# Optimization experiments

Measured on AMD Instinct MI355X. Metric: run time of the kernel, lower is better.

## Reference

```python
import jax, jax.numpy as jnp
import numpy as np

B, C, H, W = 8, 256, 128, 128
G = 32            # n_groups
CPG = C // G      # channels per group = 8
K = 3             # adaptive spatial kernel and final conv kernel
OUT = 256         # out_channels of final conv
EPS = 1e-5
DN = ('NCHW', 'OIHW', 'NCHW')


def setup_inputs() -> dict:
    key = jax.random.key(0)
    ks = jax.random.split(key, 6)
    x = jax.random.normal(ks[0], (B, C, H, W), jnp.float32)
    w_spatial = jax.random.normal(ks[1], (B, C, CPG, K, K), jnp.float32) * 0.05
    w_pointwise = jax.random.normal(ks[2], (B, C, CPG, 1, 1), jnp.float32) * 0.05
    bias = jax.random.normal(ks[3], (B, C), jnp.float32) * 0.05
    # learned params of the final (static) conv
    conv_w = jax.random.normal(ks[4], (OUT, C, K, K), jnp.float32) * 0.05
    conv_b = jax.random.normal(ks[5], (OUT,), jnp.float32) * 0.05
    return {'x': x, 'w_spatial': w_spatial, 'w_pointwise': w_pointwise,
            'bias': bias, 'conv_w': conv_w, 'conv_b': conv_b}


def _ada_single(x, ws, wp, b):
    # x: [C,H,W]; ws: [C,CPG,K,K]; wp: [C,CPG,1,1]; b: [C]
    pad = (K - 1) // 2
    xp = jnp.pad(x, ((0, 0), (pad, pad), (pad, pad)), mode='reflect')
    # grouped spatial conv (channel-preserving)
    y = jax.lax.conv_general_dilated(
        xp[None], ws, (1, 1), 'VALID',
        dimension_numbers=DN, feature_group_count=G)[0]      # [C,H,W]
    # grouped 1x1 conv as per-group small matmul
    yg = y.reshape(G, CPG, H, W)
    wg = wp[:, :, 0, 0].reshape(G, CPG, CPG)                 # [G, out/g, in/g]
    z = jnp.einsum('goi,gihw->gohw', wg, yg).reshape(C, H, W)
    return z + b[:, None, None]


def reference(x, w_spatial, w_pointwise, bias, conv_w, conv_b):
    # instance norm (no affine), biased variance as in F.instance_norm
    mean = x.mean(axis=(2, 3), keepdims=True)
    var = x.var(axis=(2, 3), keepdims=True)
    xn = (x - mean) * jax.lax.rsqrt(var + EPS)
    # per-sample adaptive depthwise-separable conv
    y = jax.vmap(_ada_single)(xn, w_spatial, w_pointwise, bias)  # [B,C,H,W]
    # final static conv, reflect padding (ceil,floor) = (1,1) for k=3
    yp = jnp.pad(y, ((0, 0), (0, 0), (1, 1), (1, 1)), mode='reflect')
    out = jax.lax.conv_general_dilated(yp, conv_w, (1, 1), 'VALID',
                                       dimension_numbers=DN)
    return out + conv_b[None, :, None, None]
```

## Files before the change

kernel.cpp:

```cpp
#include <hip/hip_runtime.h>
#include <stdint.h>
#include <stddef.h>


typedef __attribute__((ext_vector_type(8))) short   s16x8;
typedef __attribute__((ext_vector_type(4))) float   f32x4;

#define NB   8
#define NC   256
#define NH   128
#define NW   128
#define NG   32
#define CPG  8
#define NOUT 256
#define HWPLANE (NH*NW)

__device__ __forceinline__ unsigned short f2bf(float f) {
    union { float f; unsigned u; } v; v.f = f;
    unsigned u = v.u;
    u += 0x7fffu + ((u >> 16) & 1u);
    return (unsigned short)(u >> 16);
}

__device__ __forceinline__ int refl128(int i) {
    return i < 0 ? 1 : (i > 127 ? 126 : i);
}

__device__ __forceinline__ void async_load16(const void* g, void* l) {
    __builtin_amdgcn_global_load_lds(
        (const __attribute__((address_space(1))) unsigned int*)g,
        (__attribute__((address_space(3))) unsigned int*)l,
        16, 0, 0);
}

__global__ __launch_bounds__(256) void stats_k(const float* __restrict__ x,
                                               float* __restrict__ stats) {
    int bc = blockIdx.x, t = threadIdx.x;
    const float4* p = (const float4*)(x + (size_t)bc * HWPLANE);
    float s = 0.f, q = 0.f;
#pragma unroll
    for (int k = 0; k < 16; ++k) {
        float4 v = p[k * 256 + t];
        s += v.x + v.y + v.z + v.w;
        q += v.x * v.x + v.y * v.y + v.z * v.z + v.w * v.w;
    }
    __shared__ float ss[256], sq[256];
    ss[t] = s; sq[t] = q;
    __syncthreads();
    for (int o = 128; o > 0; o >>= 1) {
        if (t < o) { ss[t] += ss[t + o]; sq[t] += sq[t + o]; }
        __syncthreads();
    }
    if (t == 0) {
        float mean = ss[0] * (1.f / HWPLANE);
        float var  = sq[0] * (1.f / HWPLANE) - mean * mean;
        stats[bc * 2]     = mean;
        stats[bc * 2 + 1] = rsqrtf(var + 1e-5f);
    }
}

__global__ __launch_bounds__(256) void weff_k(const float* __restrict__ wsp,
                                              const float* __restrict__ wpw,
                                              float* __restrict__ weff) {
    int tid = blockIdx.x * 256 + threadIdx.x;
    int e  = tid % 72;
    int bc = tid / 72;
    int c = bc & 255, b = bc >> 8, g = c >> 3;
    int i = e / 9, t = e - i * 9;
    float acc = 0.f;
#pragma unroll
    for (int j = 0; j < 8; ++j)
        acc += wpw[bc * 8 + j] * wsp[(((b * NC + g * 8 + j) * CPG) + i) * 9 + t];
    weff[(size_t)bc * 72 + e] = acc;
}

__global__ __launch_bounds__(256) void repack_k(const float* __restrict__ cw,
                                                unsigned short* __restrict__ wtT) {
    int tid = blockIdx.x * 256 + threadIdx.x;
    int c = tid & 255;
    int o = (tid >> 8) & 255;
    int t = tid >> 16;
    float v = cw[(size_t)(o * NC + c) * 9 + t];
    wtT[((size_t)t * NOUT + o) * NC + c] = f2bf(v);
}

__global__ __launch_bounds__(128) void ada_k(const float* __restrict__ x,
                                             const float* __restrict__ stats,
                                             const float* __restrict__ weff,
                                             const float* __restrict__ bias,
                                             unsigned short* __restrict__ z) {
    int bx = blockIdx.x;
    int h = bx & 127;
    int g = (bx >> 7) & 31;
    int b = bx >> 12;
    int w = threadIdx.x;

    __shared__ float sx[CPG][3][NW];
#pragma unroll
    for (int ic = 0; ic < CPG; ++ic) {
        int cg = g * 8 + ic;
        float mean = stats[(b * NC + cg) * 2];
        float rstd = stats[(b * NC + cg) * 2 + 1];
        const float* xp = x + (size_t)(b * NC + cg) * HWPLANE;
#pragma unroll
        for (int dh = 0; dh < 3; ++dh) {
            int r = refl128(h + dh - 1);
            sx[ic][dh][w] = (xp[r * NW + w] - mean) * rstd;
        }
    }
    __syncthreads();

    float acc[CPG];
    const float* bp = bias + b * NC + g * 8;
#pragma unroll
    for (int c = 0; c < CPG; ++c) acc[c] = bp[c];

    const float* wp = weff + (size_t)(b * NC + g * 8) * 72;
    int wm = (w == 0) ? 1 : w - 1;
    int wq = (w == 127) ? 126 : w + 1;

#pragma unroll
    for (int ic = 0; ic < CPG; ++ic) {
        float xv[9];
#pragma unroll
        for (int dh = 0; dh < 3; ++dh) {
            xv[dh * 3 + 0] = sx[ic][dh][wm];
            xv[dh * 3 + 1] = sx[ic][dh][w];
            xv[dh * 3 + 2] = sx[ic][dh][wq];
        }
#pragma unroll
        for (int c = 0; c < CPG; ++c)
#pragma unroll
            for (int t = 0; t < 9; ++t)
                acc[c] += wp[c * 72 + ic * 9 + t] * xv[t];
    }

    unsigned short ob[8];
#pragma unroll
    for (int c = 0; c < CPG; ++c) ob[c] = f2bf(acc[c]);
    uint4 pk;
    pk.x = (unsigned)ob[0] | ((unsigned)ob[1] << 16);
    pk.y = (unsigned)ob[2] | ((unsigned)ob[3] << 16);
    pk.z = (unsigned)ob[4] | ((unsigned)ob[5] << 16);
    pk.w = (unsigned)ob[6] | ((unsigned)ob[7] << 16);
    *(uint4*)(z + ((size_t)((b * NH + h) * NW + w)) * NC + g * 8) = pk;
}

__global__ __launch_bounds__(256, 3) void final_k(const unsigned short* __restrict__ z,
                                                  const unsigned short* __restrict__ wtT,
                                                  const float* __restrict__ cb,
                                                  float* __restrict__ out) {
    __shared__ s16x8 sAv[1024];
    __shared__ s16x8 sBv[2][1024];

    const int id = blockIdx.x;
    const int b  = id & 7;
    const int jb = id >> 3;
    const int nb = jb & 1;
    const int h  = jb >> 1;

    const int tid  = threadIdx.x;
    const int wv   = tid >> 6;
    const int lane = tid & 63;
    const int l15  = lane & 15;
    const int quad = lane >> 4;
    const int mo   = (wv & 1) << 6;
    const int nol  = (wv >> 1) << 6;
    const int n0   = (nb << 7) + nol;

    int srcoff[4], ldsoff[4];
#pragma unroll
    for (int it = 0; it < 4; ++it) {
        int ch  = it * 256 + tid;
        int row = ch >> 3, cp = ch & 7;
        srcoff[it] = row * 512 + ((cp ^ (row & 7)) << 4);
        ldsoff[it] = it * 256 + wv * 64;
    }

    int aoff[3][4][2];
#pragma unroll
    for (int dw = 0; dw < 3; ++dw)
#pragma unroll
        for (int i = 0; i < 4; ++i) {
            int w_ = refl128(mo + 16 * i + l15 + dw - 1);
#pragma unroll
            for (int kk = 0; kk < 2; ++kk)
                aoff[dw][i][kk] = w_ * 8 + ((kk * 4 + quad) ^ (w_ & 7));
        }
    int boff[4][2];
#pragma unroll
    for (int j = 0; j < 4; ++j) {
        int oc_l = nol + 16 * j + l15;
#pragma unroll
        for (int kk = 0; kk < 2; ++kk)
            boff[j][kk] = oc_l * 8 + ((kk * 4 + quad) ^ (oc_l & 7));
    }

    const char* zb = (const char*)z + (size_t)b * (HWPLANE * NC * 2);
    const char* zr[3];
#pragma unroll
    for (int dh = 0; dh < 3; ++dh)
        zr[dh] = zb + (size_t)refl128(h + dh - 1) * (NW * NC * 2);
    const char* wt = (const char*)wtT + nb * 65536;

    auto stageA = [&](const char* g) {
#pragma unroll
        for (int it = 0; it < 4; ++it)
            async_load16(g + srcoff[it], (void*)(sAv + ldsoff[it]));
    };
    auto stageB = [&](const char* g, int bsel) {
#pragma unroll
        for (int it = 0; it < 4; ++it)
            async_load16(g + srcoff[it], (void*)(sBv[bsel] + ldsoff[it]));
    };

    f32x4 acc[4][4] = {};

    auto compute = [&](const int (&ao)[4][2], int bsel) {
        const s16x8* bbase = sBv[bsel];
#pragma unroll
        for (int kk = 0; kk < 2; ++kk) {
            s16x8 av[4], bv[4];
#pragma unroll
            for (int i = 0; i < 4; ++i) av[i] = sAv[ao[i][kk]];
#pragma unroll
            for (int j = 0; j < 4; ++j) bv[j] = bbase[boff[j][kk]];
#pragma unroll
            for (int i = 0; i < 4; ++i)
#pragma unroll
                for (int j = 0; j < 4; ++j)
                    acc[i][j] = __builtin_amdgcn_mfma_f32_16x16x32_bf16(
                        av[i], bv[j], acc[i][j], 0, 0, 0);
        }
    };

    int buf = 0;
    stageA(zr[0]);
    stageB(wt, 0);
    __syncthreads();

    for (int sc = 0; sc < 12; ++sc) {
        const int dh = sc >> 2, kc = sc & 3;
        const char* bt = wt + (size_t)(dh * 3) * 131072 + kc * 128;
        stageB(bt + 131072, buf ^ 1);
        compute(aoff[0], buf);
        __syncthreads(); buf ^= 1;
        stageB(bt + 262144, buf ^ 1);
        compute(aoff[1], buf);
        __syncthreads(); buf ^= 1;
        compute(aoff[2], buf);
        __syncthreads();
        if (sc < 11) {
            const int sn = sc + 1, dhn = sn >> 2, kcn = sn & 3;
            stageA(zr[dhn] + kcn * 128);
            stageB(wt + (size_t)(dhn * 3) * 131072 + kcn * 128, buf ^ 1);
            __syncthreads();
        }
        buf ^= 1;
    }

#pragma unroll
    for (int j = 0; j < 4; ++j) {
        int oc = n0 + 16 * j + l15;
        float bvl = cb[oc];
#pragma unroll
        for (int i = 0; i < 4; ++i) {
            int w0 = mo + 16 * i + quad * 4;
            float* dst = out + (((size_t)(b * NOUT + oc) * NH + h) * NW + w0);
            f32x4 v = acc[i][j];
            float4 o4 = { v[0] + bvl, v[1] + bvl, v[2] + bvl, v[3] + bvl };
            *(float4*)dst = o4;
        }
    }
}

extern "C" void kernel_launch(void* const* d_in, const int* in_sizes, int n_in,
                              void* d_out, int out_size, void* d_ws, size_t ws_size,
                              hipStream_t stream) {
    const float* x   = (const float*)d_in[0];
    const float* wsp = (const float*)d_in[1];
    const float* wpw = (const float*)d_in[2];
    const float* bia = (const float*)d_in[3];
    const float* cw  = (const float*)d_in[4];
    const float* cb  = (const float*)d_in[5];
    float* out = (float*)d_out;

    char* ws = (char*)d_ws;
    float*          stats = (float*)ws;
    float*          weff  = (float*)(ws + 16384);
    unsigned short* wtT   = (unsigned short*)(ws + 606208);
    unsigned short* z     = (unsigned short*)(ws + 1785856);

    stats_k <<<NB * NC, 256, 0, stream>>>(x, stats);
    weff_k  <<<576,     256, 0, stream>>>(wsp, wpw, weff);
    repack_k<<<2304,    256, 0, stream>>>(cw, wtT);
    ada_k   <<<NB * NG * NH, 128, 0, stream>>>(x, stats, weff, bia, z);
    final_k <<<NB * NH * 2,  256, 0, stream>>>(z, wtT, cb, out);
}
```

Measured before the change: 501.2 us.

## Tile adaptive conv over 8 rows per block with register-blocked rows and reordered weights

The adaptive grouped conv kernel now handles an 8-row tile per 256-thread block instead of one row per 128-thread block. It loads 10 halo rows into shared memory with float4 loads, and each thread computes 4 output rows for 8 output channels. Each loaded input value is reused across 3 vertical taps and 4 rows, which cuts redundant halo reads from global memory. The effective-weight layout is transposed to [ic][tap][oc] so the 8 output-channel weights are contiguous. The cost is higher register use (32 accumulators) and larger shared memory per block.

```diff
diff --git a/kernel.cpp b/kernel.cpp
--- a/kernel.cpp
+++ b/kernel.cpp
@@ -63,15 +63,17 @@
                                               const float* __restrict__ wpw,
                                               float* __restrict__ weff) {
     int tid = blockIdx.x * 256 + threadIdx.x;
-    int e  = tid % 72;
-    int bc = tid / 72;
-    int c = bc & 255, b = bc >> 8, g = c >> 3;
-    int i = e / 9, t = e - i * 9;
+    int oc = tid & 7;
+    int q  = tid >> 3;
+    int t  = q % 9;
+    int q2 = q / 9;
+    int ic = q2 & 7;
+    int bg = q2 >> 3;
     float acc = 0.f;
 #pragma unroll
     for (int j = 0; j < 8; ++j)
-        acc += wpw[bc * 8 + j] * wsp[(((b * NC + g * 8 + j) * CPG) + i) * 9 + t];
-    weff[(size_t)bc * 72 + e] = acc;
+        acc += wpw[(bg * 8 + oc) * 8 + j] * wsp[((bg * 8 + j) * 8 + ic) * 9 + t];
+    weff[(size_t)((bg * 8 + ic) * 9 + t) * 8 + oc] = acc;
 }
 
 __global__ __launch_bounds__(256) void repack_k(const float* __restrict__ cw,
@@ -84,66 +86,83 @@
     wtT[((size_t)t * NOUT + o) * NC + c] = f2bf(v);
 }
 
-__global__ __launch_bounds__(128) void ada_k(const float* __restrict__ x,
+__global__ __launch_bounds__(256) void ada_k(const float* __restrict__ x,
                                              const float* __restrict__ stats,
                                              const float* __restrict__ weff,
                                              const float* __restrict__ bias,
                                              unsigned short* __restrict__ z) {
-    int bx = blockIdx.x;
-    int h = bx & 127;
-    int g = (bx >> 7) & 31;
-    int b = bx >> 12;
-    int w = threadIdx.x;
-
-    __shared__ float sx[CPG][3][NW];
-#pragma unroll
-    for (int ic = 0; ic < CPG; ++ic) {
-        int cg = g * 8 + ic;
+    __shared__ float sx[CPG][10][NW];
+    const int bx = blockIdx.x;
+    const int ht = bx & 15;
+    const int g  = (bx >> 4) & 31;
+    const int b  = bx >> 9;
+    const int h0 = ht * 8;
+
+#pragma unroll
+    for (int it = 0; it < 10; ++it) {
+        int p   = it * 256 + threadIdx.x;
+        int ic  = p / 320;
+        int rem = p - ic * 320;
+        int row = rem >> 5;
+        int w4  = rem & 31;
+        int cg  = g * 8 + ic;
         float mean = stats[(b * NC + cg) * 2];
         float rstd = stats[(b * NC + cg) * 2 + 1];
-        const float* xp = x + (size_t)(b * NC + cg) * HWPLANE;
-#pragma unroll
-        for (int dh = 0; dh < 3; ++dh) {
-            int r = refl128(h + dh - 1);
-            sx[ic][dh][w] = (xp[r * NW + w] - mean) * rstd;
-        }
+        int rr = refl128(h0 - 1 + row);
+        const float4* xp4 = (const float4*)(x + (size_t)(b * NC + cg) * HWPLANE + rr * NW);
+        float4 v = xp4[w4];
+        float4 n = { (v.x - mean) * rstd, (v.y - mean) * rstd,
+                     (v.z - mean) * rstd, (v.w - mean) * rstd };
+        *(float4*)&sx[ic][row][w4 * 4] = n;
     }
     __syncthreads();
 
-    float acc[CPG];
-    const float* bp = bias + b * NC + g * 8;
-#pragma unroll
-    for (int c = 0; c < CPG; ++c) acc[c] = bp[c];
-
-    const float* wp = weff + (size_t)(b * NC + g * 8) * 72;
-    int wm = (w == 0) ? 1 : w - 1;
-    int wq = (w == 127) ? 126 : w + 1;
+    const int w  = threadIdx.x & 127;
+    const int hq = threadIdx.x >> 7;
+
+    const float* wbase = weff + (size_t)(b * NG + g) * 576;
+    const float* bp    = bias + b * NC + g * 8;
+
+    float acc[4][8];
+#pragma unroll
+    for (int r = 0; r < 4; ++r)
+#pragma unroll
+        for (int oc = 0; oc < 8; ++oc) acc[r][oc] = bp[oc];
 
 #pragma unroll
     for (int ic = 0; ic < CPG; ++ic) {
-        float xv[9];
-#pragma unroll
-        for (int dh = 0; dh < 3; ++dh) {
-            xv[dh * 3 + 0] = sx[ic][dh][wm];
-            xv[dh * 3 + 1] = sx[ic][dh][w];
-            xv[dh * 3 + 2] = sx[ic][dh][wq];
-        }
-#pragma unroll
-        for (int c = 0; c < CPG; ++c)
-#pragma unroll
-            for (int t = 0; t < 9; ++t)
-                acc[c] += wp[c * 72 + ic * 9 + t] * xv[t];
-    }
-
-    unsigned short ob[8];
-#pragma unroll
-    for (int c = 0; c < CPG; ++c) ob[c] = f2bf(acc[c]);
-    uint4 pk;
-    pk.x = (unsigned)ob[0] | ((unsigned)ob[1] << 16);
-    pk.y = (unsigned)ob[2] | ((unsigned)ob[3] << 16);
-    pk.z = (unsigned)ob[4] | ((unsigned)ob[5] << 16);
-    pk.w = (unsigned)ob[6] | ((unsigned)ob[7] << 16);
-    *(uint4*)(z + ((size_t)((b * NH + h) * NW + w)) * NC + g * 8) = pk;
+#pragma unroll
+        for (int dw = 0; dw < 3; ++dw) {
+            int wc = w + dw - 1;
+            wc = wc < 0 ? 1 : (wc > 127 ? 126 : wc);
+            float xr[6];
+#pragma unroll
+            for (int rr = 0; rr < 6; ++rr) xr[rr] = sx[ic][hq * 4 + rr][wc];
+#pragma unroll
+            for (int dh = 0; dh < 3; ++dh) {
+                const float* wv = wbase + (ic * 9 + dh * 3 + dw) * 8;
+#pragma unroll
+                for (int r = 0; r < 4; ++r)
+#pragma unroll
+                    for (int oc = 0; oc < 8; ++oc)
+                        acc[r][oc] += wv[oc] * xr[r + dh];
+            }
+        }
+    }
+
+#pragma unroll
+    for (int r = 0; r < 4; ++r) {
+        int h = h0 + hq * 4 + r;
+        unsigned short ob[8];
+#pragma unroll
+        for (int oc = 0; oc < 8; ++oc) ob[oc] = f2bf(acc[r][oc]);
+        uint4 pk;
+        pk.x = (unsigned)ob[0] | ((unsigned)ob[1] << 16);
+        pk.y = (unsigned)ob[2] | ((unsigned)ob[3] << 16);
+        pk.z = (unsigned)ob[4] | ((unsigned)ob[5] << 16);
+        pk.w = (unsigned)ob[6] | ((unsigned)ob[7] << 16);
+        *(uint4*)(z + (size_t)((b * NH + h) * NW + w) * NC + g * 8) = pk;
+    }
 }
 
 __global__ __launch_bounds__(256, 3) void final_k(const unsigned short* __restrict__ z,
@@ -294,6 +313,6 @@
     stats_k <<<NB * NC, 256, 0, stream>>>(x, stats);
     weff_k  <<<576,     256, 0, stream>>>(wsp, wpw, weff);
     repack_k<<<2304,    256, 0, stream>>>(cw, wtT);
-    ada_k   <<<NB * NG * NH, 128, 0, stream>>>(x, stats, weff, bia, z);
+    ada_k   <<<NB * NG * (NH / 8), 256, 0, stream>>>(x, stats, weff, bia, z);
     final_k <<<NB * NH * 2,  256, 0, stream>>>(z, wtT, cb, out);
 }
```

New measurement: 434.0 us. -13.4%, faster.
